# Optimization experiments

Measured on AMD Instinct MI355X. Metric: run time of the kernel, lower is better.

Reference implementation:

```python
import jax, jax.numpy as jnp
from jax import lax
import numpy as np

STRIDE = 16
PRE_NMS = 2000
POST_NMS = 300
NMS_THRESH = 0.7
MIN_SIZE = 16.0  # * img_scale (=1.0)
DN = ('NCHW', 'OIHW', 'NCHW')


def _anchor_base(base=16, ratios=(0.5, 1.0, 2.0), scales=(8, 16, 32)):
    py = px = base / 2.0
    ab = np.zeros((len(ratios) * len(scales), 4), np.float32)
    k = 0
    for r in ratios:
        for s in scales:
            h = base * s * np.sqrt(r)
            w = base * s * np.sqrt(1.0 / r)
            ab[k] = [py - h / 2, px - w / 2, py + h / 2, px + w / 2]
            k += 1
    return ab


def _all_anchors(H, W, img_h, img_w):
    base = _anchor_base()
    sy = np.arange(H, dtype=np.float32) * STRIDE
    sx = np.arange(W, dtype=np.float32) * STRIDE
    yy, xx = np.meshgrid(sy, sx, indexing='ij')
    shifts = np.stack([yy, xx, yy, xx], axis=-1).reshape(-1, 1, 4)
    anchors = (shifts + base[None]).reshape(-1, 4).astype(np.float32)  # (H*W*9, 4)
    valid = np.where((anchors[:, 0] >= 0) & (anchors[:, 1] >= 0) &
                     (anchors[:, 2] <= img_h) & (anchors[:, 3] <= img_w))[0]
    return anchors, valid


def _loc2bbox(anc, loc):
    # anc: (1,K,4), loc: (B,K,4); boxes as (y1,x1,y2,x2)
    h = anc[..., 2] - anc[..., 0]
    w = anc[..., 3] - anc[..., 1]
    cy = anc[..., 0] + 0.5 * h
    cx = anc[..., 1] + 0.5 * w
    ncy = loc[..., 0] * h + cy
    ncx = loc[..., 1] * w + cx
    nh = h * jnp.exp(loc[..., 2])
    nw = w * jnp.exp(loc[..., 3])
    return jnp.stack([ncy - 0.5 * nh, ncx - 0.5 * nw,
                      ncy + 0.5 * nh, ncx + 0.5 * nw], axis=-1)


def _nms(boxes, scores):
    # boxes: (N,4), scores: (N,) -> (POST_NMS,4) zero-padded rois
    areas = (boxes[:, 2] - boxes[:, 0]) * (boxes[:, 3] - boxes[:, 1])

    def step(s, _):
        i = jnp.argmax(s)
        ok = s[i] > -jnp.inf
        b = boxes[i]
        yy1 = jnp.maximum(b[0], boxes[:, 0])
        xx1 = jnp.maximum(b[1], boxes[:, 1])
        yy2 = jnp.minimum(b[2], boxes[:, 2])
        xx2 = jnp.minimum(b[3], boxes[:, 3])
        inter = jnp.maximum(yy2 - yy1, 0.0) * jnp.maximum(xx2 - xx1, 0.0)
        iou = inter / (areas[i] + areas - inter + 1e-9)
        s = jnp.where(iou > NMS_THRESH, -jnp.inf, s).at[i].set(-jnp.inf)
        return s, (i, ok)

    _, (idx, ok) = lax.scan(step, scores, None, length=POST_NMS)
    return boxes[idx] * ok[:, None].astype(boxes.dtype)


def _conv(x, w, b, padding):
    y = lax.conv_general_dilated(x, w, (1, 1), padding, dimension_numbers=DN)
    return y + b[None, :, None, None]


def setup_inputs():
    key = jax.random.key(0)
    k = jax.random.split(key, 4)
    B, C, H, W = 2, 512, 64, 64
    std = 0.01
    return {
        'feat': jax.random.normal(k[0], (B, C, H, W), jnp.float32),
        'share_w': jax.random.normal(k[1], (512, 512, 3, 3), jnp.float32) * std,
        'share_b': jnp.zeros((512,), jnp.float32),
        'cls_w': jax.random.normal(k[2], (18, 512, 1, 1), jnp.float32) * std,
        'cls_b': jnp.zeros((18,), jnp.float32),
        'reg_w': jax.random.normal(k[3], (36, 512, 1, 1), jnp.float32) * std,
        'reg_b': jnp.zeros((36,), jnp.float32),
        'img_h': 1024,
        'img_w': 1024,
    }


def reference(feat, share_w, share_b, cls_w, cls_b, reg_w, reg_b, img_h, img_w):
    B, _, H, W = feat.shape
    anchors_np, valid_np = _all_anchors(H, W, img_h, img_w)
    anchors = jnp.asarray(anchors_np)
    valid = jnp.asarray(valid_np)

    shared = jax.nn.relu(_conv(feat, share_w, share_b, 'SAME'))
    cls = _conv(shared, cls_w, cls_b, 'VALID')   # (B,18,H,W)
    reg = _conv(shared, reg_w, reg_b, 'VALID')   # (B,36,H,W)

    # permute(0,2,3,1).view(-1,2), gather valid anchors, softmax
    cls = cls.transpose(0, 2, 3, 1).reshape(B, -1, 2)[:, valid]   # (B,K,2)
    cls = jax.nn.softmax(cls, axis=-1)
    reg = reg.transpose(0, 2, 3, 1).reshape(B, -1, 4)[:, valid]   # (B,K,4)

    # proposal layer: decode, clip, min-size filter, top-k, NMS
    anc = anchors[valid][None]                                    # (1,K,4)
    boxes = _loc2bbox(anc, reg)                                   # (B,K,4)
    boxes = jnp.stack([jnp.clip(boxes[..., 0], 0.0, img_h),
                       jnp.clip(boxes[..., 1], 0.0, img_w),
                       jnp.clip(boxes[..., 2], 0.0, img_h),
                       jnp.clip(boxes[..., 3], 0.0, img_w)], axis=-1)
    hs = boxes[..., 2] - boxes[..., 0]
    ws = boxes[..., 3] - boxes[..., 1]
    scores = jnp.where((hs >= MIN_SIZE) & (ws >= MIN_SIZE), cls[..., 1], -jnp.inf)

    top_s, top_i = lax.top_k(scores, PRE_NMS)                     # (B,PRE_NMS)
    top_boxes = jnp.take_along_axis(boxes, top_i[..., None], axis=1)
    rois = jax.vmap(_nms)(top_boxes, top_s)                       # (B,POST_NMS,4)
    roi_list = rois.reshape(-1, 4)
    roi_id = jnp.repeat(jnp.arange(B, dtype=jnp.int32), POST_NMS)
    return cls, reg, roi_list, roi_id, anchors
```

## Files before the change

### kernel.cpp

```cpp
#include <hip/hip_runtime.h>
#include <math.h>

typedef unsigned int u32;
typedef unsigned long long u64;
typedef unsigned short ushort_t;

typedef __attribute__((ext_vector_type(8))) short short8;
typedef __attribute__((ext_vector_type(16))) float f32x16;

#define KANC 18376
#define PRE 2000
#define PREP 2048
#define POST 300

#define OUT_CLS 0
#define OUT_REG 73504
#define OUT_ROI 220512
#define OUT_RID 222912
#define OUT_ANC 223512

#define WS_NHWC   0u
#define WS_FT     16777216u
#define WS_W3     41943040u
#define WS_VPOS   56098816u
#define WS_BOXES  56246272u
#define WS_KEYS   56834304u
#define WS_TOPBOX 56981312u
#define WS_TOPKEY 57046848u
#define WS_MASK   57063232u

#define A_SPL2 7920

__device__ __forceinline__ ushort_t f2bf(float f) {
    u32 u = __float_as_uint(f);
    u32 r = (u + 0x7FFFu + ((u >> 16) & 1u)) >> 16;
    return (ushort_t)r;
}
__device__ __forceinline__ float bf2f(ushort_t h) {
    return __uint_as_float(((u32)h) << 16);
}
__device__ __forceinline__ u32 pack3(float v0, float v1, ushort_t* m0, ushort_t* m1,
                                     ushort_t* l0, ushort_t* l1) {
    ushort_t h0 = f2bf(v0);
    float r = v0 - bf2f(h0);
    *m0 = f2bf(r);
    *l0 = f2bf(r - bf2f(*m0));
    ushort_t h1 = f2bf(v1);
    float r1 = v1 - bf2f(h1);
    *m1 = f2bf(r1);
    *l1 = f2bf(r1 - bf2f(*m1));
    return (u32)h0 | ((u32)h1 << 16);
}

__device__ __forceinline__ void anchor_base(int t, float& y1, float& x1, float& y2, float& x2) {
    const double SQ[3] = {0.7071067811865476, 1.0, 1.4142135623730951};
    const double SC[3] = {8.0, 16.0, 32.0};
    int ri = t / 3, si = t % 3;
    double h = 16.0 * SC[si] * SQ[ri];
    double w = 16.0 * SC[si] * SQ[2 - ri];
    y1 = (float)(8.0 - h * 0.5);
    x1 = (float)(8.0 - w * 0.5);
    y2 = (float)(8.0 + h * 0.5);
    x2 = (float)(8.0 + w * 0.5);
}

__global__ __launch_bounds__(256) void t12_pre(const float* __restrict__ feat,
                                               const float* __restrict__ w,
                                               ushort_t* __restrict__ ft,
                                               ushort_t* __restrict__ w3,
                                               float* __restrict__ nhwc) {
    __shared__ float lds[8 * 577];
    int tid = threadIdx.x;
    int bid = blockIdx.x;
    if (bid < 1024) {
        float4 z4 = make_float4(0.f, 0.f, 0.f, 0.f);
        float4* nz = (float4*)nhwc + (size_t)bid * 1024;
        for (int i = tid; i < 1024; i += 256) nz[i] = z4;

        int by = bid >> 3;
        int b = by >> 6, y = by & 63;
        int ci0 = (bid & 7) * 64;
        for (int it = 0; it < 16; it++) {
            int idx = it * 256 + tid;
            int ci = idx >> 6, x = idx & 63;
            lds[ci * 65 + x] = feat[((size_t)(b * 512 + ci0 + ci) * 64 + y) * 64 + x];
        }
        __syncthreads();
        const size_t spl = (size_t)2 * 64 * 64 * 512;
        u32* ft32 = (u32*)ft;
        for (int it = 0; it < 8; it++) {
            int idx = it * 256 + tid;
            int x = idx >> 5, cp = idx & 31;
            float v0 = lds[(2 * cp) * 65 + x];
            float v1 = lds[(2 * cp + 1) * 65 + x];
            ushort_t m0, m1, l0, l1;
            u32 hi = pack3(v0, v1, &m0, &m1, &l0, &l1);
            size_t base = ((size_t)(b * 64 + y) * 64 + x) * 512 + ci0 + 2 * cp;
            ft32[base >> 1] = hi;
            ft32[(base + spl) >> 1] = (u32)m0 | ((u32)m1 << 16);
            ft32[(base + 2 * spl) >> 1] = (u32)l0 | ((u32)l1 << 16);
        }
    } else {
        int b2 = bid - 1024;
        int cob = b2 >> 3;
        int cib = (b2 & 7) * 64;
        for (int s = tid; s < 4608; s += 256) {
            int co = s / 576, r = s - co * 576;
            lds[co * 577 + r] = w[((size_t)(cob * 8 + co) * 512 + cib) * 9 + r];
        }
        __syncthreads();
        const size_t spl = (size_t)9 * 512 * 512;
        u32* w32 = (u32*)w3;
        int co = tid >> 5, cp = tid & 31;
        for (int kk = 0; kk < 9; kk++) {
            float v0 = lds[co * 577 + (2 * cp) * 9 + kk];
            float v1 = lds[co * 577 + (2 * cp + 1) * 9 + kk];
            ushort_t m0, m1, l0, l1;
            u32 hi = pack3(v0, v1, &m0, &m1, &l0, &l1);
            size_t base = ((size_t)kk * 512 + cob * 8 + co) * 512 + cib + 2 * cp;
            w32[base >> 1] = hi;
            w32[(base + spl) >> 1] = (u32)m0 | ((u32)m1 << 16);
            w32[(base + 2 * spl) >> 1] = (u32)l0 | ((u32)l1 << 16);
        }
    }
}

__global__ __launch_bounds__(256, 2) void k1_conv(const ushort_t* __restrict__ ft,
                                                  const ushort_t* __restrict__ w3,
                                                  float* __restrict__ nhwc) {
    __shared__ ushort_t lds16[3 * A_SPL2];
    int tid = threadIdx.x;
    int bid = blockIdx.x;
    int nt = (bid >> 1) & 1;
    int kh = (bid >> 2) & 1;
    int mt = ((bid >> 3) << 1) | (bid & 1);
    int b = mt >> 6, y = mt & 63;
    int nb = nt << 8;
    int ct0 = kh * 8;

    int lane = tid & 63;
    int w = tid >> 6;
    int wn = w << 6;
    int nlane = lane & 31;
    int kgrp8 = (lane >> 5) * 8;

    const size_t FT_SPL = (size_t)2 * 64 * 64 * 512;
    const size_t W3_SPL = (size_t)9 * 512 * 512;

    int sx = tid >> 2;
    int sq = tid & 3;

    f32x16 acc[2];
    f32x16 acc2[2];
#pragma unroll
    for (int ni = 0; ni < 2; ni++)
#pragma unroll
        for (int r = 0; r < 16; r++) { acc[ni][r] = 0.0f; acc2[ni][r] = 0.0f; }

    if (tid < 72) {
        int s = tid / 24, rem = tid % 24;
        int r = rem >> 3, rem2 = rem & 7;
        int side = rem2 >> 2, q = rem2 & 3;
        uint4 z = make_uint4(0, 0, 0, 0);
        *(uint4*)&lds16[s * A_SPL2 + (r * 66 + side * 65) * 40 + q * 8] = z;
    }

    uint4 pbA[9];
    auto loadA = [&](int ct) {
#pragma unroll
        for (int r = 0; r < 3; r++) {
            int yy = y - 1 + r;
            bool valid = (yy >= 0 && yy < 64);
            size_t rowbase = ((size_t)(b * 64 + (valid ? yy : 0)) * 64 + sx) * 512 + ct * 32 + sq * 8;
#pragma unroll
            for (int s = 0; s < 3; s++) {
                uint4 v = make_uint4(0, 0, 0, 0);
                if (valid) v = *(const uint4*)&ft[rowbase + (size_t)s * FT_SPL];
                pbA[r * 3 + s] = v;
            }
        }
    };
    auto writeA = [&]() {
#pragma unroll
        for (int r = 0; r < 3; r++)
#pragma unroll
            for (int s = 0; s < 3; s++)
                *(uint4*)&lds16[s * A_SPL2 + (r * 66 + sx + 1) * 40 + sq * 8] = pbA[r * 3 + s];
    };

    short8 breg[2][2][3];
    auto loadB = [&](int buf, int tap, int ks, int ct) {
#pragma unroll
        for (int ni = 0; ni < 2; ni++) {
            size_t cobase = ((size_t)(tap * 512 + nb + wn + ni * 32 + nlane)) * 512
                            + ct * 32 + ks * 16 + kgrp8;
#pragma unroll
            for (int s = 0; s < 3; s++)
                breg[buf][ni][s] = *(const short8*)&w3[(size_t)s * W3_SPL + cobase];
        }
    };

    loadA(ct0);
    loadB(0, 0, 0, ct0);

    for (int ct = ct0; ct < ct0 + 8; ct++) {
        __syncthreads();
        writeA();
        __syncthreads();
        if (ct + 1 < ct0 + 8) loadA(ct + 1);

#pragma unroll
        for (int u = 0; u < 18; u++) {
            int cur = u & 1, alt = cur ^ 1;
            if (u + 1 < 18) loadB(alt, (u + 1) >> 1, (u + 1) & 1, ct);
            else if (ct + 1 < ct0 + 8) loadB(alt, 0, 0, ct + 1);
            int tap = u >> 1, ks = u & 1;
            int ky = tap / 3, kx = tap - ky * 3;

            short8 af[3][2];
#pragma unroll
            for (int s = 0; s < 3; s++) {
#pragma unroll
                for (int mi = 0; mi < 2; mi++)
                    af[s][mi] = *(const short8*)&lds16[s * A_SPL2 +
                        (ky * 66 + mi * 32 + nlane + kx) * 40 + ks * 16 + kgrp8];
            }
#pragma unroll
            for (int t = 0; t < 6; t++) {
                const int sa_t[6] = {0, 0, 1, 0, 1, 2};
                const int sb_t[6] = {0, 1, 0, 2, 1, 0};
                int sa = sa_t[t], sb = sb_t[t];
#pragma unroll
                for (int ni = 0; ni < 2; ni++) {
                    acc[ni]  = __builtin_amdgcn_mfma_f32_32x32x16_bf16(
                        af[sa][0], breg[cur][ni][sb], acc[ni], 0, 0, 0);
                    acc2[ni] = __builtin_amdgcn_mfma_f32_32x32x16_bf16(
                        af[sa][1], breg[cur][ni][sb], acc2[ni], 0, 0, 0);
                }
            }
        }
    }

#pragma unroll
    for (int ni = 0; ni < 2; ni++) {
        int co = nb + wn + ni * 32 + nlane;
#pragma unroll
        for (int r = 0; r < 16; r++) {
            int xx = (r & 3) + 8 * (r >> 2) + 4 * (lane >> 5);
            atomicAdd(&nhwc[((size_t)(b * 64 + y) * 64 + xx) * 512 + co], acc[ni][r]);
            atomicAdd(&nhwc[((size_t)(b * 64 + y) * 64 + 32 + xx) * 512 + co], acc2[ni][r]);
        }
    }
}

__global__ __launch_bounds__(256) void k2_heads(const float* __restrict__ nhwc,
                                                const float* __restrict__ share_b,
                                                const float* __restrict__ cls_w,
                                                const float* __restrict__ cls_b,
                                                const float* __restrict__ reg_w,
                                                const float* __restrict__ reg_b,
                                                float* __restrict__ out,
                                                float* __restrict__ boxes_ws,
                                                u32* __restrict__ keys_ws,
                                                const int* d_imgh, const int* d_imgw) {
    int bid = blockIdx.x;
    int row = bid >> 2;
    int b = row >> 6, y = row & 63;
    int q = bid & 3;
    int p0 = q * 16;
    int tid = threadIdx.x;
    __shared__ float Al[16 * 68];
    __shared__ float Wl[64 * 64];
    __shared__ float Ob[54 * 16];
    int og = tid & 15, pg = tid >> 4;
    float acc[4];
#pragma unroll
    for (int j = 0; j < 4; j++) acc[j] = 0.0f;

    for (int cib = 0; cib < 512; cib += 64) {
        for (int s = tid; s < 1024; s += 256) {
            int kk = s & 63, pp = s >> 6;
            float v = nhwc[((size_t)(b * 64 + y) * 64 + p0 + pp) * 512 + cib + kk]
                      + share_b[cib + kk];
            Al[pp * 68 + kk] = fmaxf(v, 0.0f);
        }
        for (int s = tid; s < 64 * 64; s += 256) {
            int o = s >> 6, kk = s & 63;
            float wv = 0.0f;
            if (o < 18) wv = cls_w[o * 512 + cib + kk];
            else if (o < 54) wv = reg_w[(o - 18) * 512 + cib + kk];
            Wl[s] = wv;
        }
        __syncthreads();
        for (int kq = 0; kq < 16; kq++) {
            float4 a4 = *(const float4*)&Al[pg * 68 + kq * 4];
#pragma unroll
            for (int j = 0; j < 4; j++) {
                float4 w4 = *(const float4*)&Wl[(og * 4 + j) * 64 + kq * 4];
                acc[j] += a4.x * w4.x + a4.y * w4.y + a4.z * w4.z + a4.w * w4.w;
            }
        }
        __syncthreads();
    }
#pragma unroll
    for (int j = 0; j < 4; j++) {
        int o = og * 4 + j;
        if (o < 54) {
            float bvv = (o < 18) ? cls_b[o] : reg_b[o - 18];
            Ob[o * 16 + pg] = acc[j] + bvv;
        }
    }
    __syncthreads();
    float imgh = (float)d_imgh[0], imgw = (float)d_imgw[0];
    for (int task = tid; task < 144; task += 256) {
        int ta = task >> 4, p2 = task & 15;
        int x = p0 + p2;
        int a_idx = (y * 64 + x) * 9 + ta;
        int j = 0;
        bool myvalid = false;
#pragma unroll
        for (int tt = 0; tt < 9; tt++) {
            float c0, c1, c2, c3;
            anchor_base(tt, c0, c1, c2, c3);
            int ylo = (int)((-c0) / 16.0f) + 1;
            int yhi = (int)((imgh - c2) / 16.0f);
            int xlo = (int)((-c1) / 16.0f) + 1;
            int xhi = (int)((imgw - c3) / 16.0f);
            ylo = max(ylo, 0); yhi = min(yhi, 63);
            xlo = max(xlo, 0); xhi = min(xhi, 63);
            int Wt  = max(xhi - xlo + 1, 0);
            int nry = max(yhi - ylo + 1, 0);
            int rb  = min(max(y - ylo, 0), nry);
            bool vy = (y >= ylo) && (y <= yhi);
            int cb  = vy ? min(max(x - xlo, 0), Wt) : 0;
            bool val = vy && (x >= xlo) && (x <= xhi);
            j += rb * Wt + cb + ((tt < ta && val) ? 1 : 0);
            if (tt == ta) {
                myvalid = val;
                float4 o4;
                o4.x = c0 + 16.0f * y;
                o4.y = c1 + 16.0f * x;
                o4.z = c2 + 16.0f * y;
                o4.w = c3 + 16.0f * x;
                *(float4*)&out[OUT_ANC + a_idx * 4] = o4;
            }
        }
        if (!myvalid) continue;
        float c0 = Ob[(2 * ta) * 16 + p2], c1 = Ob[(2 * ta + 1) * 16 + p2];
        float m = fmaxf(c0, c1);
        float e0 = expf(c0 - m), e1 = expf(c1 - m);
        float sden = e0 + e1;
        float p0v = e0 / sden, p1v = e1 / sden;
        out[OUT_CLS + (size_t)(b * KANC + j) * 2 + 0] = p0v;
        out[OUT_CLS + (size_t)(b * KANC + j) * 2 + 1] = p1v;
        float l0 = Ob[(18 + 4 * ta + 0) * 16 + p2];
        float l1 = Ob[(18 + 4 * ta + 1) * 16 + p2];
        float l2 = Ob[(18 + 4 * ta + 2) * 16 + p2];
        float l3 = Ob[(18 + 4 * ta + 3) * 16 + p2];
        out[OUT_REG + (size_t)(b * KANC + j) * 4 + 0] = l0;
        out[OUT_REG + (size_t)(b * KANC + j) * 4 + 1] = l1;
        out[OUT_REG + (size_t)(b * KANC + j) * 4 + 2] = l2;
        out[OUT_REG + (size_t)(b * KANC + j) * 4 + 3] = l3;
        float b0, b1, b2, b3; anchor_base(ta, b0, b1, b2, b3);
        float ay1 = b0 + 16.0f * y, ax1 = b1 + 16.0f * x;
        float ay2 = b2 + 16.0f * y, ax2 = b3 + 16.0f * x;
        float hh = ay2 - ay1, wdt = ax2 - ax1;
        float cy = ay1 + 0.5f * hh, cx = ax1 + 0.5f * wdt;
        float ncy = l0 * hh + cy, ncx = l1 * wdt + cx;
        float nh = hh * expf(l2), nw = wdt * expf(l3);
        float by1 = fminf(fmaxf(ncy - 0.5f * nh, 0.0f), imgh);
        float bx1 = fminf(fmaxf(ncx - 0.5f * nw, 0.0f), imgw);
        float by2 = fminf(fmaxf(ncy + 0.5f * nh, 0.0f), imgh);
        float bx2 = fminf(fmaxf(ncx + 0.5f * nw, 0.0f), imgw);
        boxes_ws[(size_t)(b * KANC + j) * 4 + 0] = by1;
        boxes_ws[(size_t)(b * KANC + j) * 4 + 1] = bx1;
        boxes_ws[(size_t)(b * KANC + j) * 4 + 2] = by2;
        boxes_ws[(size_t)(b * KANC + j) * 4 + 3] = bx2;
        float hs = by2 - by1, wsz = bx2 - bx1;
        u32 key = 0;
        if (hs >= 16.0f && wsz >= 16.0f) key = __float_as_uint(p1v) + 1u;
        keys_ws[b * KANC + j] = key;
    }
}

__device__ __forceinline__ void suffix_scan(u32* suf, const u32* hist, int N, int tid) {
    for (int i = tid; i < N; i += 1024) suf[i] = hist[i];
    if (tid == 0) suf[N] = 0;
    __syncthreads();
    for (int off = 1; off < N; off <<= 1) {
        u32 add0 = 0, add1 = 0;
        int i0 = tid, i1 = tid + 1024;
        if (i0 < N) add0 = (i0 + off < N) ? suf[i0 + off] : 0;
        if (i1 < N) add1 = (i1 + off < N) ? suf[i1 + off] : 0;
        __syncthreads();
        if (i0 < N) suf[i0] += add0;
        if (i1 < N) suf[i1] += add1;
        __syncthreads();
    }
}

__global__ __launch_bounds__(1024) void k3_select(const u32* __restrict__ keys_ws,
                                                  const float* __restrict__ boxes_ws,
                                                  u32* __restrict__ topkey,
                                                  float* __restrict__ topbox) {
    int b = blockIdx.x, tid = threadIdx.x;
    const u32* keys = keys_ws + (size_t)b * KANC;
    __shared__ u64 sbuf[2048];
    __shared__ u32 hist[2048];
    __shared__ u32 suf[2049];
    __shared__ int Ps;
    __shared__ int cnt;

    u32* hist_p = (u32*)sbuf;
    int cpy = tid >> 7;
    for (int i = tid; i < 4096; i += 1024) hist_p[i] = 0;
    __syncthreads();
    for (int i = tid; i < KANC; i += 1024) atomicAdd(&hist_p[cpy * 512 + (keys[i] >> 22)], 1u);
    __syncthreads();
    for (int bin = tid; bin < 512; bin += 1024) {
        u32 s = 0;
#pragma unroll
        for (int c = 0; c < 8; c++) s += hist_p[c * 512 + bin];
        hist[bin] = s;
    }
    __syncthreads();
    suffix_scan(suf, hist, 512, tid);
    if (tid == 0) Ps = 0;
    __syncthreads();
    for (int i = tid; i < 512; i += 1024)
        if (suf[i] >= (u32)PRE && suf[i + 1] < (u32)PRE) Ps = i;
    __syncthreads();
    u32 P1 = (u32)Ps;
    u32 quota2 = (u32)PRE - suf[P1 + 1];
    __syncthreads();

    for (int i = tid; i < 2048; i += 1024) hist[i] = 0;
    __syncthreads();
    for (int i = tid; i < KANC; i += 1024) {
        u32 k = keys[i];
        if ((k >> 22) == P1) atomicAdd(&hist[(k >> 11) & 2047u], 1u);
    }
    __syncthreads();
    suffix_scan(suf, hist, 2048, tid);
    if (tid == 0) Ps = 0;
    __syncthreads();
    for (int i = tid; i < 2048; i += 1024)
        if (suf[i] >= quota2 && suf[i + 1] < quota2) Ps = i;
    __syncthreads();
    u32 P2 = (u32)Ps;
    u32 quota3 = quota2 - suf[P2 + 1];
    __syncthreads();

    u32 pref = (P1 << 11) | P2;
    for (int i = tid; i < 2048; i += 1024) hist[i] = 0;
    __syncthreads();
    for (int i = tid; i < KANC; i += 1024) {
        u32 k = keys[i];
        if ((k >> 11) == pref) atomicAdd(&hist[k & 2047u], 1u);
    }
    __syncthreads();
    suffix_scan(suf, hist, 2048, tid);
    if (tid == 0) Ps = 0;
    __syncthreads();
    for (int i = tid; i < 2048; i += 1024)
        if (suf[i] >= quota3 && suf[i + 1] < quota3) Ps = i;
    __syncthreads();
    u32 P3 = (u32)Ps;
    u32 T = (P1 << 22) | (P2 << 11) | P3;
    u32 Tm = (T < 1u) ? 1u : T;

    __syncthreads();
    for (int i = tid; i < 2048; i += 1024) sbuf[i] = 0ull;
    if (tid == 0) cnt = 0;
    __syncthreads();
    int lane = tid & 63;
    for (int i = tid; i < KANC + 1023; i += 1024) {
        u32 k = (i < KANC) ? keys[i] : 0u;
        bool p = (i < KANC) && (k >= Tm);
        u64 m = __ballot(p);
        if (m) {
            int ldr = __ffsll((unsigned long long)m) - 1;
            int base = 0;
            if (lane == ldr) base = atomicAdd(&cnt, __popcll(m));
            base = __shfl(base, ldr);
            if (p) {
                int pos = base + __popcll(m & ((1ull << lane) - 1ull));
                if (pos < 2048)
                    sbuf[pos] = ((u64)k << 32) | (u64)(0xFFFFFFFFu - (u32)i);
            }
        }
    }
    __syncthreads();

    for (int k2 = 2; k2 <= 2048; k2 <<= 1) {
        for (int j2 = k2 >> 1; j2 > 0; j2 >>= 1) {
            for (int i = tid; i < 2048; i += 1024) {
                int ixj = i ^ j2;
                if (ixj > i) {
                    u64 va = sbuf[i], vb = sbuf[ixj];
                    bool descRegion = ((i & k2) == 0);
                    if (descRegion ? (va < vb) : (va > vb)) {
                        sbuf[i] = vb; sbuf[ixj] = va;
                    }
                }
            }
            __syncthreads();
        }
    }

    for (int i = tid; i < PREP; i += 1024) {
        u64 v = sbuf[i];
        u32 kk = (u32)(v >> 32);
        u32 j = 0xFFFFFFFFu - (u32)(v & 0xFFFFFFFFull);
        bool good = (i < PRE) && (kk != 0);
        topkey[b * PREP + i] = good ? kk : 0;
        float4 bx = make_float4(0.0f, 0.0f, 0.0f, 0.0f);
        if (good) bx = *(const float4*)&boxes_ws[(size_t)(b * KANC + j) * 4];
        *(float4*)&topbox[(size_t)(b * PREP + i) * 4] = bx;
    }
}

__global__ __launch_bounds__(256) void k4_mask(const float* __restrict__ topbox,
                                               u64* __restrict__ mask) {
    int ib = blockIdx.y, b = blockIdx.z;
    int lane = threadIdx.x & 63;
    int jb = blockIdx.x * 4 + (threadIdx.x >> 6);
    if (jb < ib) {
        mask[(size_t)(b * PREP + ib * 64 + lane) * 32 + jb] = 0ull;
        return;
    }
    float4 bi = *(const float4*)&topbox[(size_t)(b * PREP + ib * 64 + lane) * 4];
    float4 bj = *(const float4*)&topbox[(size_t)(b * PREP + jb * 64 + lane) * 4];
    float ai = (bi.z - bi.x) * (bi.w - bi.y);
    float aj = (bj.z - bj.x) * (bj.w - bj.y);
    u64 word = 0;
    for (int ii = 0; ii < 64; ii++) {
        float y1 = __shfl(bi.x, ii), x1 = __shfl(bi.y, ii);
        float y2 = __shfl(bi.z, ii), x2 = __shfl(bi.w, ii);
        float aii = __shfl(ai, ii);
        float yy1 = fmaxf(y1, bj.x), xx1 = fmaxf(x1, bj.y);
        float yy2 = fminf(y2, bj.z), xx2 = fminf(x2, bj.w);
        float inter = fmaxf(yy2 - yy1, 0.0f) * fmaxf(xx2 - xx1, 0.0f);
        float iou = inter / (aii + aj - inter + 1e-9f);
        u64 bal = __ballot(iou > 0.7f);
        if (lane == ii) word = bal;
    }
    mask[(size_t)(b * PREP + ib * 64 + lane) * 32 + jb] = word;
}

__global__ __launch_bounds__(64) void k5_nms(const u32* __restrict__ topkey,
                                             const float* __restrict__ topbox,
                                             const u64* __restrict__ mask,
                                             float* __restrict__ out) {
    int b = blockIdx.x;
    int lane = threadIdx.x;
    __shared__ int kept[POST];

    u64 validw = 0;
    for (int it = 0; it < 32; it++) {
        u64 wv = __ballot(topkey[b * PREP + it * 64 + lane] != 0);
        if (lane == it) validw = wv;
    }

    const u64* mb = mask + (size_t)b * PREP * 32;
    u64 remv = 0;
    const int CH = 16;
    u64 bufA[CH], bufB[CH];
    auto loadRows = [&](u64* buf, int base) {
#pragma unroll
        for (int k = 0; k < CH; k++)
            buf[k] = (lane < 32) ? mb[(size_t)(base + k) * 32 + lane] : 0ull;
    };
    int nk = 0;
    auto process = [&](u64* buf, int base) {
        int wi = base >> 6, sh = base & 63;
        u64 supw = __shfl(remv, wi);
        u64 valw = __shfl(validw, wi);
        u32 cand = (u32)(((~supw & valw) >> sh) & 0xFFFFull);
        while (cand) {
            int k = __builtin_ctz(cand);
            cand &= cand - 1;
            int i = base + k;
            remv |= buf[k];
            u64 rw = __shfl(buf[k], wi);
            cand &= ~((u32)((rw >> sh) & 0xFFFFull));
            if (lane == 0) kept[nk] = i;
            nk++;
            if (nk == POST) break;
        }
    };

    loadRows(bufA, 0);
    for (int base = 0; base < PRE && nk < POST; base += 2 * CH) {
        loadRows(bufB, base + CH);
        process(bufA, base);
        if (nk < POST && base + CH < PRE) {
            if (base + 2 * CH < PRE) loadRows(bufA, base + 2 * CH);
            process(bufB, base + CH);
        }
    }
    __syncthreads();
    for (int s = lane; s < POST; s += 64) {
        float4 bx = make_float4(0.0f, 0.0f, 0.0f, 0.0f);
        if (s < nk) bx = *(const float4*)&topbox[(size_t)(b * PREP + kept[s]) * 4];
        *(float4*)&out[OUT_ROI + (size_t)(b * POST + s) * 4] = bx;
        out[OUT_RID + b * POST + s] = (float)b;
    }
}

extern "C" void kernel_launch(void* const* d_in, const int* in_sizes, int n_in,
                              void* d_out, int out_size, void* d_ws, size_t ws_size,
                              hipStream_t stream) {
    (void)in_sizes; (void)n_in; (void)out_size; (void)ws_size;
    const float* feat    = (const float*)d_in[0];
    const float* share_w = (const float*)d_in[1];
    const float* share_b = (const float*)d_in[2];
    const float* cls_w   = (const float*)d_in[3];
    const float* cls_b   = (const float*)d_in[4];
    const float* reg_w   = (const float*)d_in[5];
    const float* reg_b   = (const float*)d_in[6];
    const int*   imgh    = (const int*)d_in[7];
    const int*   imgw    = (const int*)d_in[8];
    float* out = (float*)d_out;
    char* ws = (char*)d_ws;
    float*     nhwc   = (float*)(ws + WS_NHWC);
    ushort_t*  ft     = (ushort_t*)(ws + WS_FT);
    ushort_t*  w3     = (ushort_t*)(ws + WS_W3);
    float*     boxes  = (float*)(ws + WS_BOXES);
    u32*       keys   = (u32*)(ws + WS_KEYS);
    float*     topbox = (float*)(ws + WS_TOPBOX);
    u32*       topkey = (u32*)(ws + WS_TOPKEY);
    u64*       maskp  = (u64*)(ws + WS_MASK);

    t12_pre<<<1536, 256, 0, stream>>>(feat, share_w, ft, w3, nhwc);
    k1_conv<<<512, 256, 0, stream>>>(ft, w3, nhwc);
    k2_heads<<<512, 256, 0, stream>>>(nhwc, share_b, cls_w, cls_b, reg_w, reg_b,
                                      out, boxes, keys, imgh, imgw);
    k3_select<<<2, 1024, 0, stream>>>(keys, boxes, topkey, topbox);
    k4_mask<<<dim3(8, 32, 2), 256, 0, stream>>>(topbox, maskp);
    k5_nms<<<2, 64, 0, stream>>>(topkey, topbox, maskp, out);
}
```

Measured before the change: 646.1 us.

## Fuse all six RPN stages into one cooperative persistent kernel with grid syncs

Merges the pre-pack, conv, heads, top-k select, IoU mask and NMS kernels into a single cooperative kernel of 512 blocks, with grid.sync between stages. The aim is to remove the launch gaps between six kernels. In exchange, top-k selection runs on 2 blocks of 256 threads instead of 1024, the pre-pass packs two units per block, and the other blocks sit idle at each grid barrier. If the cooperative launch fails, the code falls back to the original six-kernel sequence.

Measured after the change: 1.036 ms. 1.6x slower.

```diff
diff --git a/kernel.cpp b/kernel.cpp
--- a/kernel.cpp
+++ b/kernel.cpp
@@ -1,5 +1,8 @@
 #include <hip/hip_runtime.h>
+#include <hip/hip_cooperative_groups.h>
 #include <math.h>
+
+namespace cg = cooperative_groups;
 
 typedef unsigned int u32;
 typedef unsigned long long u64;
@@ -30,6 +33,7 @@
 #define WS_MASK   57063232u
 
 #define A_SPL2 7920
+#define SMEM_BYTES 47520
 
 __device__ __forceinline__ ushort_t f2bf(float f) {
     u32 u = __float_as_uint(f);
@@ -63,6 +67,547 @@
     y2 = (float)(8.0 + h * 0.5);
     x2 = (float)(8.0 + w * 0.5);
 }
+
+__device__ __forceinline__ void suffix_scan256(u32* suf, const u32* hist, int N, int tid) {
+    for (int i = tid; i < N; i += 256) suf[i] = hist[i];
+    if (tid == 0) suf[N] = 0;
+    __syncthreads();
+    for (int off = 1; off < N; off <<= 1) {
+        u32 add[8];
+        int c = 0;
+        for (int i = tid; i < N; i += 256) { add[c++] = (i + off < N) ? suf[i + off] : 0; }
+        __syncthreads();
+        c = 0;
+        for (int i = tid; i < N; i += 256) { suf[i] += add[c++]; }
+        __syncthreads();
+    }
+}
+
+__global__ __launch_bounds__(256, 2) void mega(
+    const float* __restrict__ feat, const float* __restrict__ share_w,
+    const float* __restrict__ share_b, const float* __restrict__ cls_w,
+    const float* __restrict__ cls_b, const float* __restrict__ reg_w,
+    const float* __restrict__ reg_b, const int* __restrict__ d_imgh,
+    const int* __restrict__ d_imgw, float* __restrict__ out,
+    float* __restrict__ nhwc, ushort_t* __restrict__ ft,
+    ushort_t* __restrict__ w3, float* __restrict__ boxes_ws,
+    u32* __restrict__ keys_ws, float* __restrict__ topbox,
+    u32* __restrict__ topkey, u64* __restrict__ maskp)
+{
+    __shared__ __align__(16) unsigned char smem[SMEM_BYTES];
+    cg::grid_group grid = cg::this_grid();
+    int tid = threadIdx.x;
+    int bid = blockIdx.x;
+
+    {
+        float* lds = (float*)smem;
+        for (int fu = 0; fu < 2; fu++) {
+            int u = bid * 2 + fu;
+            float4 z4 = make_float4(0.f, 0.f, 0.f, 0.f);
+            float4* nz = (float4*)nhwc + (size_t)u * 1024;
+            for (int i = tid; i < 1024; i += 256) nz[i] = z4;
+            int by = u >> 3; int b = by >> 6, y = by & 63;
+            int ci0 = (u & 7) * 64;
+            for (int it = 0; it < 16; it++) {
+                int idx = it * 256 + tid;
+                int ci = idx >> 6, x = idx & 63;
+                lds[ci * 65 + x] = feat[((size_t)(b * 512 + ci0 + ci) * 64 + y) * 64 + x];
+            }
+            __syncthreads();
+            const size_t spl = (size_t)2 * 64 * 64 * 512;
+            u32* ft32 = (u32*)ft;
+            for (int it = 0; it < 8; it++) {
+                int idx = it * 256 + tid;
+                int x = idx >> 5, cp = idx & 31;
+                float v0 = lds[(2 * cp) * 65 + x];
+                float v1 = lds[(2 * cp + 1) * 65 + x];
+                ushort_t m0, m1, l0, l1;
+                u32 hi = pack3(v0, v1, &m0, &m1, &l0, &l1);
+                size_t base = ((size_t)(b * 64 + y) * 64 + x) * 512 + ci0 + 2 * cp;
+                ft32[base >> 1] = hi;
+                ft32[(base + spl) >> 1] = (u32)m0 | ((u32)m1 << 16);
+                ft32[(base + 2 * spl) >> 1] = (u32)l0 | ((u32)l1 << 16);
+            }
+            __syncthreads();
+        }
+        {
+            int cob = bid >> 3, cib = (bid & 7) * 64;
+            for (int s = tid; s < 4608; s += 256) {
+                int co = s / 576, r = s - co * 576;
+                lds[co * 577 + r] = share_w[((size_t)(cob * 8 + co) * 512 + cib) * 9 + r];
+            }
+            __syncthreads();
+            const size_t spl = (size_t)9 * 512 * 512;
+            u32* w32 = (u32*)w3;
+            int co = tid >> 5, cp = tid & 31;
+            for (int kk = 0; kk < 9; kk++) {
+                float v0 = lds[co * 577 + (2 * cp) * 9 + kk];
+                float v1 = lds[co * 577 + (2 * cp + 1) * 9 + kk];
+                ushort_t m0, m1, l0, l1;
+                u32 hi = pack3(v0, v1, &m0, &m1, &l0, &l1);
+                size_t base = ((size_t)kk * 512 + cob * 8 + co) * 512 + cib + 2 * cp;
+                w32[base >> 1] = hi;
+                w32[(base + spl) >> 1] = (u32)m0 | ((u32)m1 << 16);
+                w32[(base + 2 * spl) >> 1] = (u32)l0 | ((u32)l1 << 16);
+            }
+        }
+    }
+    grid.sync();
+
+    {
+        ushort_t* lds16 = (ushort_t*)smem;
+        int nt = (bid >> 1) & 1;
+        int kh = (bid >> 2) & 1;
+        int mt = ((bid >> 3) << 1) | (bid & 1);
+        int b = mt >> 6, y = mt & 63;
+        int nb = nt << 8;
+        int ct0 = kh * 8;
+
+        int lane = tid & 63;
+        int w = tid >> 6;
+        int wn = w << 6;
+        int nlane = lane & 31;
+        int kgrp8 = (lane >> 5) * 8;
+
+        const size_t FT_SPL = (size_t)2 * 64 * 64 * 512;
+        const size_t W3_SPL = (size_t)9 * 512 * 512;
+
+        int sx = tid >> 2;
+        int sq = tid & 3;
+
+        f32x16 acc[2];
+        f32x16 acc2[2];
+#pragma unroll
+        for (int ni = 0; ni < 2; ni++)
+#pragma unroll
+            for (int r = 0; r < 16; r++) { acc[ni][r] = 0.0f; acc2[ni][r] = 0.0f; }
+
+        if (tid < 72) {
+            int s = tid / 24, rem = tid % 24;
+            int r = rem >> 3, rem2 = rem & 7;
+            int side = rem2 >> 2, q = rem2 & 3;
+            uint4 z = make_uint4(0, 0, 0, 0);
+            *(uint4*)&lds16[s * A_SPL2 + (r * 66 + side * 65) * 40 + q * 8] = z;
+        }
+
+        uint4 pbA[9];
+        auto loadA = [&](int ct) {
+#pragma unroll
+            for (int r = 0; r < 3; r++) {
+                int yy = y - 1 + r;
+                bool valid = (yy >= 0 && yy < 64);
+                size_t rowbase = ((size_t)(b * 64 + (valid ? yy : 0)) * 64 + sx) * 512 + ct * 32 + sq * 8;
+#pragma unroll
+                for (int s = 0; s < 3; s++) {
+                    uint4 v = make_uint4(0, 0, 0, 0);
+                    if (valid) v = *(const uint4*)&ft[rowbase + (size_t)s * FT_SPL];
+                    pbA[r * 3 + s] = v;
+                }
+            }
+        };
+        auto writeA = [&]() {
+#pragma unroll
+            for (int r = 0; r < 3; r++)
+#pragma unroll
+                for (int s = 0; s < 3; s++)
+                    *(uint4*)&lds16[s * A_SPL2 + (r * 66 + sx + 1) * 40 + sq * 8] = pbA[r * 3 + s];
+        };
+
+        short8 breg[2][2][3];
+        auto loadB = [&](int buf, int tap, int ks, int ct) {
+#pragma unroll
+            for (int ni = 0; ni < 2; ni++) {
+                size_t cobase = ((size_t)(tap * 512 + nb + wn + ni * 32 + nlane)) * 512
+                                + ct * 32 + ks * 16 + kgrp8;
+#pragma unroll
+                for (int s = 0; s < 3; s++)
+                    breg[buf][ni][s] = *(const short8*)&w3[(size_t)s * W3_SPL + cobase];
+            }
+        };
+
+        loadA(ct0);
+        loadB(0, 0, 0, ct0);
+
+        for (int ct = ct0; ct < ct0 + 8; ct++) {
+            __syncthreads();
+            writeA();
+            __syncthreads();
+            if (ct + 1 < ct0 + 8) loadA(ct + 1);
+
+#pragma unroll
+            for (int u = 0; u < 18; u++) {
+                int cur = u & 1, alt = cur ^ 1;
+                if (u + 1 < 18) loadB(alt, (u + 1) >> 1, (u + 1) & 1, ct);
+                else if (ct + 1 < ct0 + 8) loadB(alt, 0, 0, ct + 1);
+                int tap = u >> 1, ks = u & 1;
+                int ky = tap / 3, kx = tap - ky * 3;
+
+                short8 af[3][2];
+#pragma unroll
+                for (int s = 0; s < 3; s++) {
+#pragma unroll
+                    for (int mi = 0; mi < 2; mi++)
+                        af[s][mi] = *(const short8*)&lds16[s * A_SPL2 +
+                            (ky * 66 + mi * 32 + nlane + kx) * 40 + ks * 16 + kgrp8];
+                }
+#pragma unroll
+                for (int t = 0; t < 6; t++) {
+                    const int sa_t[6] = {0, 0, 1, 0, 1, 2};
+                    const int sb_t[6] = {0, 1, 0, 2, 1, 0};
+                    int sa = sa_t[t], sb = sb_t[t];
+#pragma unroll
+                    for (int ni = 0; ni < 2; ni++) {
+                        acc[ni]  = __builtin_amdgcn_mfma_f32_32x32x16_bf16(
+                            af[sa][0], breg[cur][ni][sb], acc[ni], 0, 0, 0);
+                        acc2[ni] = __builtin_amdgcn_mfma_f32_32x32x16_bf16(
+                            af[sa][1], breg[cur][ni][sb], acc2[ni], 0, 0, 0);
+                    }
+                }
+            }
+        }
+
+#pragma unroll
+        for (int ni = 0; ni < 2; ni++) {
+            int co = nb + wn + ni * 32 + nlane;
+#pragma unroll
+            for (int r = 0; r < 16; r++) {
+                int xx = (r & 3) + 8 * (r >> 2) + 4 * (lane >> 5);
+                atomicAdd(&nhwc[((size_t)(b * 64 + y) * 64 + xx) * 512 + co], acc[ni][r]);
+                atomicAdd(&nhwc[((size_t)(b * 64 + y) * 64 + 32 + xx) * 512 + co], acc2[ni][r]);
+            }
+        }
+    }
+    grid.sync();
+
+    {
+        int row = bid >> 2;
+        int b = row >> 6, y = row & 63;
+        int q = bid & 3;
+        int p0 = q * 16;
+        float* Al = (float*)smem;
+        float* Wl = Al + 16 * 68;
+        float* Ob = Wl + 64 * 64;
+        int og = tid & 15, pg = tid >> 4;
+        float acc[4];
+#pragma unroll
+        for (int j = 0; j < 4; j++) acc[j] = 0.0f;
+
+        for (int cib = 0; cib < 512; cib += 64) {
+            for (int s = tid; s < 1024; s += 256) {
+                int kk = s & 63, pp = s >> 6;
+                float v = nhwc[((size_t)(b * 64 + y) * 64 + p0 + pp) * 512 + cib + kk]
+                          + share_b[cib + kk];
+                Al[pp * 68 + kk] = fmaxf(v, 0.0f);
+            }
+            for (int s = tid; s < 64 * 64; s += 256) {
+                int o = s >> 6, kk = s & 63;
+                float wv = 0.0f;
+                if (o < 18) wv = cls_w[o * 512 + cib + kk];
+                else if (o < 54) wv = reg_w[(o - 18) * 512 + cib + kk];
+                Wl[s] = wv;
+            }
+            __syncthreads();
+            for (int kq = 0; kq < 16; kq++) {
+                float4 a4 = *(const float4*)&Al[pg * 68 + kq * 4];
+#pragma unroll
+                for (int j = 0; j < 4; j++) {
+                    float4 w4 = *(const float4*)&Wl[(og * 4 + j) * 64 + kq * 4];
+                    acc[j] += a4.x * w4.x + a4.y * w4.y + a4.z * w4.z + a4.w * w4.w;
+                }
+            }
+            __syncthreads();
+        }
+#pragma unroll
+        for (int j = 0; j < 4; j++) {
+            int o = og * 4 + j;
+            if (o < 54) {
+                float bvv = (o < 18) ? cls_b[o] : reg_b[o - 18];
+                Ob[o * 16 + pg] = acc[j] + bvv;
+            }
+        }
+        __syncthreads();
+        float imgh = (float)d_imgh[0], imgw = (float)d_imgw[0];
+        for (int task = tid; task < 144; task += 256) {
+            int ta = task >> 4, p2 = task & 15;
+            int x = p0 + p2;
+            int a_idx = (y * 64 + x) * 9 + ta;
+            int j = 0;
+            bool myvalid = false;
+#pragma unroll
+            for (int tt = 0; tt < 9; tt++) {
+                float c0, c1, c2, c3;
+                anchor_base(tt, c0, c1, c2, c3);
+                int ylo = (int)((-c0) / 16.0f) + 1;
+                int yhi = (int)((imgh - c2) / 16.0f);
+                int xlo = (int)((-c1) / 16.0f) + 1;
+                int xhi = (int)((imgw - c3) / 16.0f);
+                ylo = max(ylo, 0); yhi = min(yhi, 63);
+                xlo = max(xlo, 0); xhi = min(xhi, 63);
+                int Wt  = max(xhi - xlo + 1, 0);
+                int nry = max(yhi - ylo + 1, 0);
+                int rb  = min(max(y - ylo, 0), nry);
+                bool vy = (y >= ylo) && (y <= yhi);
+                int cb  = vy ? min(max(x - xlo, 0), Wt) : 0;
+                bool val = vy && (x >= xlo) && (x <= xhi);
+                j += rb * Wt + cb + ((tt < ta && val) ? 1 : 0);
+                if (tt == ta) {
+                    myvalid = val;
+                    float4 o4;
+                    o4.x = c0 + 16.0f * y;
+                    o4.y = c1 + 16.0f * x;
+                    o4.z = c2 + 16.0f * y;
+                    o4.w = c3 + 16.0f * x;
+                    *(float4*)&out[OUT_ANC + a_idx * 4] = o4;
+                }
+            }
+            if (!myvalid) continue;
+            float c0 = Ob[(2 * ta) * 16 + p2], c1 = Ob[(2 * ta + 1) * 16 + p2];
+            float m = fmaxf(c0, c1);
+            float e0 = expf(c0 - m), e1 = expf(c1 - m);
+            float sden = e0 + e1;
+            float p0v = e0 / sden, p1v = e1 / sden;
+            out[OUT_CLS + (size_t)(b * KANC + j) * 2 + 0] = p0v;
+            out[OUT_CLS + (size_t)(b * KANC + j) * 2 + 1] = p1v;
+            float l0 = Ob[(18 + 4 * ta + 0) * 16 + p2];
+            float l1 = Ob[(18 + 4 * ta + 1) * 16 + p2];
+            float l2 = Ob[(18 + 4 * ta + 2) * 16 + p2];
+            float l3 = Ob[(18 + 4 * ta + 3) * 16 + p2];
+            out[OUT_REG + (size_t)(b * KANC + j) * 4 + 0] = l0;
+            out[OUT_REG + (size_t)(b * KANC + j) * 4 + 1] = l1;
+            out[OUT_REG + (size_t)(b * KANC + j) * 4 + 2] = l2;
+            out[OUT_REG + (size_t)(b * KANC + j) * 4 + 3] = l3;
+            float b0, b1, b2, b3; anchor_base(ta, b0, b1, b2, b3);
+            float ay1 = b0 + 16.0f * y, ax1 = b1 + 16.0f * x;
+            float ay2 = b2 + 16.0f * y, ax2 = b3 + 16.0f * x;
+            float hh = ay2 - ay1, wdt = ax2 - ax1;
+            float cy = ay1 + 0.5f * hh, cx = ax1 + 0.5f * wdt;
+            float ncy = l0 * hh + cy, ncx = l1 * wdt + cx;
+            float nh = hh * expf(l2), nw = wdt * expf(l3);
+            float by1 = fminf(fmaxf(ncy - 0.5f * nh, 0.0f), imgh);
+            float bx1 = fminf(fmaxf(ncx - 0.5f * nw, 0.0f), imgw);
+            float by2 = fminf(fmaxf(ncy + 0.5f * nh, 0.0f), imgh);
+            float bx2 = fminf(fmaxf(ncx + 0.5f * nw, 0.0f), imgw);
+            boxes_ws[(size_t)(b * KANC + j) * 4 + 0] = by1;
+            boxes_ws[(size_t)(b * KANC + j) * 4 + 1] = bx1;
+            boxes_ws[(size_t)(b * KANC + j) * 4 + 2] = by2;
+            boxes_ws[(size_t)(b * KANC + j) * 4 + 3] = bx2;
+            float hs = by2 - by1, wsz = bx2 - bx1;
+            u32 key = 0;
+            if (hs >= 16.0f && wsz >= 16.0f) key = __float_as_uint(p1v) + 1u;
+            keys_ws[b * KANC + j] = key;
+        }
+    }
+    grid.sync();
+
+    if (bid < 2) {
+        int b = bid;
+        const u32* keys = keys_ws + (size_t)b * KANC;
+        u64* sbuf = (u64*)smem;
+        u32* hist = (u32*)(smem + 16384);
+        u32* suf  = (u32*)(smem + 24576);
+        int* PsP  = (int*)(smem + 32784);
+        int* cntP = (int*)(smem + 32792);
+
+        u32* hist_p = (u32*)sbuf;
+        int cpy = tid >> 5;
+        for (int i = tid; i < 4096; i += 256) hist_p[i] = 0;
+        __syncthreads();
+        for (int i = tid; i < KANC; i += 256) atomicAdd(&hist_p[cpy * 512 + (keys[i] >> 22)], 1u);
+        __syncthreads();
+        for (int bin = tid; bin < 512; bin += 256) {
+            u32 s = 0;
+#pragma unroll
+            for (int c = 0; c < 8; c++) s += hist_p[c * 512 + bin];
+            hist[bin] = s;
+        }
+        __syncthreads();
+        suffix_scan256(suf, hist, 512, tid);
+        if (tid == 0) *PsP = 0;
+        __syncthreads();
+        for (int i = tid; i < 512; i += 256)
+            if (suf[i] >= (u32)PRE && suf[i + 1] < (u32)PRE) *PsP = i;
+        __syncthreads();
+        u32 P1 = (u32)*PsP;
+        u32 quota2 = (u32)PRE - suf[P1 + 1];
+        __syncthreads();
+
+        for (int i = tid; i < 2048; i += 256) hist[i] = 0;
+        __syncthreads();
+        for (int i = tid; i < KANC; i += 256) {
+            u32 k = keys[i];
+            if ((k >> 22) == P1) atomicAdd(&hist[(k >> 11) & 2047u], 1u);
+        }
+        __syncthreads();
+        suffix_scan256(suf, hist, 2048, tid);
+        if (tid == 0) *PsP = 0;
+        __syncthreads();
+        for (int i = tid; i < 2048; i += 256)
+            if (suf[i] >= quota2 && suf[i + 1] < quota2) *PsP = i;
+        __syncthreads();
+        u32 P2 = (u32)*PsP;
+        u32 quota3 = quota2 - suf[P2 + 1];
+        __syncthreads();
+
+        u32 pref = (P1 << 11) | P2;
+        for (int i = tid; i < 2048; i += 256) hist[i] = 0;
+        __syncthreads();
+        for (int i = tid; i < KANC; i += 256) {
+            u32 k = keys[i];
+            if ((k >> 11) == pref) atomicAdd(&hist[k & 2047u], 1u);
+        }
+        __syncthreads();
+        suffix_scan256(suf, hist, 2048, tid);
+        if (tid == 0) *PsP = 0;
+        __syncthreads();
+        for (int i = tid; i < 2048; i += 256)
+            if (suf[i] >= quota3 && suf[i + 1] < quota3) *PsP = i;
+        __syncthreads();
+        u32 P3 = (u32)*PsP;
+        u32 T = (P1 << 22) | (P2 << 11) | P3;
+        u32 Tm = (T < 1u) ? 1u : T;
+
+        __syncthreads();
+        for (int i = tid; i < 2048; i += 256) sbuf[i] = 0ull;
+        if (tid == 0) *cntP = 0;
+        __syncthreads();
+        int lane = tid & 63;
+        for (int i = tid; i < KANC + 255; i += 256) {
+            u32 k = (i < KANC) ? keys[i] : 0u;
+            bool p = (i < KANC) && (k >= Tm);
+            u64 m = __ballot(p);
+            if (m) {
+                int ldr = __ffsll((unsigned long long)m) - 1;
+                int base = 0;
+                if (lane == ldr) base = atomicAdd(cntP, __popcll(m));
+                base = __shfl(base, ldr);
+                if (p) {
+                    int pos = base + __popcll(m & ((1ull << lane) - 1ull));
+                    if (pos < 2048)
+                        sbuf[pos] = ((u64)k << 32) | (u64)(0xFFFFFFFFu - (u32)i);
+                }
+            }
+        }
+        __syncthreads();
+
+        for (int k2 = 2; k2 <= 2048; k2 <<= 1) {
+            for (int j2 = k2 >> 1; j2 > 0; j2 >>= 1) {
+                for (int i = tid; i < 2048; i += 256) {
+                    int ixj = i ^ j2;
+                    if (ixj > i) {
+                        u64 va = sbuf[i], vb = sbuf[ixj];
+                        bool descRegion = ((i & k2) == 0);
+                        if (descRegion ? (va < vb) : (va > vb)) {
+                            sbuf[i] = vb; sbuf[ixj] = va;
+                        }
+                    }
+                }
+                __syncthreads();
+            }
+        }
+
+        for (int i = tid; i < PREP; i += 256) {
+            u64 v = sbuf[i];
+            u32 kk = (u32)(v >> 32);
+            u32 j = 0xFFFFFFFFu - (u32)(v & 0xFFFFFFFFull);
+            bool good = (i < PRE) && (kk != 0);
+            topkey[b * PREP + i] = good ? kk : 0;
+            float4 bx = make_float4(0.0f, 0.0f, 0.0f, 0.0f);
+            if (good) bx = *(const float4*)&boxes_ws[(size_t)(b * KANC + j) * 4];
+            *(float4*)&topbox[(size_t)(b * PREP + i) * 4] = bx;
+        }
+    }
+    grid.sync();
+
+    {
+        int w = tid >> 6, lane = tid & 63;
+        int unit = bid * 4 + w;
+        int b = unit >> 10;
+        int ib = (unit >> 5) & 31;
+        int jb = unit & 31;
+        if (jb < ib) {
+            maskp[(size_t)(b * PREP + ib * 64 + lane) * 32 + jb] = 0ull;
+        } else {
+            float4 bi = *(const float4*)&topbox[(size_t)(b * PREP + ib * 64 + lane) * 4];
+            float4 bj = *(const float4*)&topbox[(size_t)(b * PREP + jb * 64 + lane) * 4];
+            float ai = (bi.z - bi.x) * (bi.w - bi.y);
+            float aj = (bj.z - bj.x) * (bj.w - bj.y);
+            u64 word = 0;
+            for (int ii = 0; ii < 64; ii++) {
+                float y1 = __shfl(bi.x, ii), x1 = __shfl(bi.y, ii);
+                float y2 = __shfl(bi.z, ii), x2 = __shfl(bi.w, ii);
+                float aii = __shfl(ai, ii);
+                float yy1 = fmaxf(y1, bj.x), xx1 = fmaxf(x1, bj.y);
+                float yy2 = fminf(y2, bj.z), xx2 = fminf(x2, bj.w);
+                float inter = fmaxf(yy2 - yy1, 0.0f) * fmaxf(xx2 - xx1, 0.0f);
+                float iou = inter / (aii + aj - inter + 1e-9f);
+                u64 bal = __ballot(iou > 0.7f);
+                if (lane == ii) word = bal;
+            }
+            maskp[(size_t)(b * PREP + ib * 64 + lane) * 32 + jb] = word;
+        }
+    }
+    grid.sync();
+
+    if (bid < 2) {
+        int b = bid;
+        int* keptL = (int*)smem;
+        int* nkP = (int*)(smem + 1280);
+        if (tid < 64) {
+            int lane = tid;
+            u64 validw = 0;
+            for (int it = 0; it < 32; it++) {
+                u64 wv = __ballot(topkey[b * PREP + it * 64 + lane] != 0);
+                if (lane == it) validw = wv;
+            }
+            const u64* mb = maskp + (size_t)b * PREP * 32;
+            u64 remv = 0;
+            const int CH = 16;
+            u64 bufA[CH], bufB[CH];
+            auto loadRows = [&](u64* buf, int base) {
+#pragma unroll
+                for (int k = 0; k < CH; k++)
+                    buf[k] = (lane < 32) ? mb[(size_t)(base + k) * 32 + lane] : 0ull;
+            };
+            int nk = 0;
+            auto process = [&](u64* buf, int base) {
+                int wi = base >> 6, sh = base & 63;
+                u64 supw = __shfl(remv, wi);
+                u64 valw = __shfl(validw, wi);
+                u32 cand = (u32)(((~supw & valw) >> sh) & 0xFFFFull);
+                while (cand) {
+                    int k = __builtin_ctz(cand);
+                    cand &= cand - 1;
+                    int i = base + k;
+                    remv |= buf[k];
+                    u64 rw = __shfl(buf[k], wi);
+                    cand &= ~((u32)((rw >> sh) & 0xFFFFull));
+                    if (lane == 0) keptL[nk] = i;
+                    nk++;
+                    if (nk == POST) break;
+                }
+            };
+            loadRows(bufA, 0);
+            for (int base = 0; base < PRE && nk < POST; base += 2 * CH) {
+                loadRows(bufB, base + CH);
+                process(bufA, base);
+                if (nk < POST && base + CH < PRE) {
+                    if (base + 2 * CH < PRE) loadRows(bufA, base + 2 * CH);
+                    process(bufB, base + CH);
+                }
+            }
+            if (lane == 0) *nkP = nk;
+        }
+        __syncthreads();
+        int nk = *nkP;
+        for (int s = tid; s < POST; s += 256) {
+            float4 bx = make_float4(0.0f, 0.0f, 0.0f, 0.0f);
+            if (s < nk) bx = *(const float4*)&topbox[(size_t)(b * PREP + keptL[s]) * 4];
+            *(float4*)&out[OUT_ROI + (size_t)(b * POST + s) * 4] = bx;
+            out[OUT_RID + b * POST + s] = (float)b;
+        }
+    }
+}
+
 
 __global__ __launch_bounds__(256) void t12_pre(const float* __restrict__ feat,
                                                const float* __restrict__ w,
@@ -76,7 +621,6 @@
         float4 z4 = make_float4(0.f, 0.f, 0.f, 0.f);
         float4* nz = (float4*)nhwc + (size_t)bid * 1024;
         for (int i = tid; i < 1024; i += 256) nz[i] = z4;
-
         int by = bid >> 3;
         int b = by >> 6, y = by & 63;
         int ci0 = (bid & 7) * 64;
@@ -137,26 +681,21 @@
     int b = mt >> 6, y = mt & 63;
     int nb = nt << 8;
     int ct0 = kh * 8;
-
     int lane = tid & 63;
     int w = tid >> 6;
     int wn = w << 6;
     int nlane = lane & 31;
     int kgrp8 = (lane >> 5) * 8;
-
     const size_t FT_SPL = (size_t)2 * 64 * 64 * 512;
     const size_t W3_SPL = (size_t)9 * 512 * 512;
-
     int sx = tid >> 2;
     int sq = tid & 3;
-
     f32x16 acc[2];
     f32x16 acc2[2];
 #pragma unroll
     for (int ni = 0; ni < 2; ni++)
 #pragma unroll
         for (int r = 0; r < 16; r++) { acc[ni][r] = 0.0f; acc2[ni][r] = 0.0f; }
-
     if (tid < 72) {
         int s = tid / 24, rem = tid % 24;
         int r = rem >> 3, rem2 = rem & 7;
@@ -164,7 +703,6 @@
         uint4 z = make_uint4(0, 0, 0, 0);
         *(uint4*)&lds16[s * A_SPL2 + (r * 66 + side * 65) * 40 + q * 8] = z;
     }
-
     uint4 pbA[9];
     auto loadA = [&](int ct) {
 #pragma unroll
@@ -187,7 +725,6 @@
             for (int s = 0; s < 3; s++)
                 *(uint4*)&lds16[s * A_SPL2 + (r * 66 + sx + 1) * 40 + sq * 8] = pbA[r * 3 + s];
     };
-
     short8 breg[2][2][3];
     auto loadB = [&](int buf, int tap, int ks, int ct) {
 #pragma unroll
@@ -199,16 +736,13 @@
                 breg[buf][ni][s] = *(const short8*)&w3[(size_t)s * W3_SPL + cobase];
         }
     };
-
     loadA(ct0);
     loadB(0, 0, 0, ct0);
-
     for (int ct = ct0; ct < ct0 + 8; ct++) {
         __syncthreads();
         writeA();
         __syncthreads();
         if (ct + 1 < ct0 + 8) loadA(ct + 1);
-
 #pragma unroll
         for (int u = 0; u < 18; u++) {
             int cur = u & 1, alt = cur ^ 1;
@@ -216,7 +750,6 @@
             else if (ct + 1 < ct0 + 8) loadB(alt, 0, 0, ct + 1);
             int tap = u >> 1, ks = u & 1;
             int ky = tap / 3, kx = tap - ky * 3;
-
             short8 af[3][2];
 #pragma unroll
             for (int s = 0; s < 3; s++) {
@@ -240,7 +773,6 @@
             }
         }
     }
-
 #pragma unroll
     for (int ni = 0; ni < 2; ni++) {
         int co = nb + wn + ni * 32 + nlane;
@@ -276,7 +808,6 @@
     float acc[4];
 #pragma unroll
     for (int j = 0; j < 4; j++) acc[j] = 0.0f;
-
     for (int cib = 0; cib < 512; cib += 64) {
         for (int s = tid; s < 1024; s += 256) {
             int kk = s & 63, pp = s >> 6;
@@ -410,7 +941,6 @@
     __shared__ u32 suf[2049];
     __shared__ int Ps;
     __shared__ int cnt;
-
     u32* hist_p = (u32*)sbuf;
     int cpy = tid >> 7;
     for (int i = tid; i < 4096; i += 1024) hist_p[i] = 0;
@@ -433,7 +963,6 @@
     u32 P1 = (u32)Ps;
     u32 quota2 = (u32)PRE - suf[P1 + 1];
     __syncthreads();
-
     for (int i = tid; i < 2048; i += 1024) hist[i] = 0;
     __syncthreads();
     for (int i = tid; i < KANC; i += 1024) {
@@ -450,7 +979,6 @@
     u32 P2 = (u32)Ps;
     u32 quota3 = quota2 - suf[P2 + 1];
     __syncthreads();
-
     u32 pref = (P1 << 11) | P2;
     for (int i = tid; i < 2048; i += 1024) hist[i] = 0;
     __syncthreads();
@@ -468,7 +996,6 @@
     u32 P3 = (u32)Ps;
     u32 T = (P1 << 22) | (P2 << 11) | P3;
     u32 Tm = (T < 1u) ? 1u : T;
-
     __syncthreads();
     for (int i = tid; i < 2048; i += 1024) sbuf[i] = 0ull;
     if (tid == 0) cnt = 0;
@@ -491,7 +1018,6 @@
         }
     }
     __syncthreads();
-
     for (int k2 = 2; k2 <= 2048; k2 <<= 1) {
         for (int j2 = k2 >> 1; j2 > 0; j2 >>= 1) {
             for (int i = tid; i < 2048; i += 1024) {
@@ -507,7 +1033,6 @@
             __syncthreads();
         }
     }
-
     for (int i = tid; i < PREP; i += 1024) {
         u64 v = sbuf[i];
         u32 kk = (u32)(v >> 32);
@@ -555,13 +1080,11 @@
     int b = blockIdx.x;
     int lane = threadIdx.x;
     __shared__ int kept[POST];
-
     u64 validw = 0;
     for (int it = 0; it < 32; it++) {
         u64 wv = __ballot(topkey[b * PREP + it * 64 + lane] != 0);
         if (lane == it) validw = wv;
     }
-
     const u64* mb = mask + (size_t)b * PREP * 32;
     u64 remv = 0;
     const int CH = 16;
@@ -589,7 +1112,6 @@
             if (nk == POST) break;
         }
     };
-
     loadRows(bufA, 0);
     for (int base = 0; base < PRE && nk < POST; base += 2 * CH) {
         loadRows(bufB, base + CH);
@@ -632,11 +1154,22 @@
     u32*       topkey = (u32*)(ws + WS_TOPKEY);
     u64*       maskp  = (u64*)(ws + WS_MASK);
 
-    t12_pre<<<1536, 256, 0, stream>>>(feat, share_w, ft, w3, nhwc);
-    k1_conv<<<512, 256, 0, stream>>>(ft, w3, nhwc);
-    k2_heads<<<512, 256, 0, stream>>>(nhwc, share_b, cls_w, cls_b, reg_w, reg_b,
-                                      out, boxes, keys, imgh, imgw);
-    k3_select<<<2, 1024, 0, stream>>>(keys, boxes, topkey, topbox);
-    k4_mask<<<dim3(8, 32, 2), 256, 0, stream>>>(topbox, maskp);
-    k5_nms<<<2, 64, 0, stream>>>(topkey, topbox, maskp, out);
-}
+    void* kargs[] = {
+        (void*)&feat, (void*)&share_w, (void*)&share_b, (void*)&cls_w,
+        (void*)&cls_b, (void*)&reg_w, (void*)&reg_b, (void*)&imgh,
+        (void*)&imgw, (void*)&out, (void*)&nhwc, (void*)&ft, (void*)&w3,
+        (void*)&boxes, (void*)&keys, (void*)&topbox, (void*)&topkey,
+        (void*)&maskp
+    };
+    hipError_t err = hipLaunchCooperativeKernel((const void*)mega, dim3(512), dim3(256),
+                                                kargs, 0, stream);
+    if (err != hipSuccess) {
+        t12_pre<<<1536, 256, 0, stream>>>(feat, share_w, ft, w3, nhwc);
+        k1_conv<<<512, 256, 0, stream>>>(ft, w3, nhwc);
+        k2_heads<<<512, 256, 0, stream>>>(nhwc, share_b, cls_w, cls_b, reg_w, reg_b,
+                                          out, boxes, keys, imgh, imgw);
+        k3_select<<<2, 1024, 0, stream>>>(keys, boxes, topkey, topbox);
+        k4_mask<<<dim3(8, 32, 2), 256, 0, stream>>>(topbox, maskp);
+        k5_nms<<<2, 64, 0, stream>>>(topkey, topbox, maskp, out);
+    }
+}
```
